# Optimization experiments

Measured on AMD Instinct MI355X. Metric: run time of the kernel, lower is better.

The kernel has to match this reference:

```python
import jax, jax.numpy as jnp
import numpy as np

DN = ('NCHW', 'OIHW', 'NCHW')
EPS = 1e-5

def _conv(x, w, stride, padding):
    return jax.lax.conv_general_dilated(x, w, stride, padding, dimension_numbers=DN)

def _bn(x, g, b, m, v):
    # inference-mode BatchNorm2d
    s = g * jax.lax.rsqrt(v + EPS)
    return x * s[None, :, None, None] + (b - m * s)[None, :, None, None]

def _gn(x, g, b, groups):
    B, C, H, W = x.shape
    xr = x.reshape(B, groups, -1)
    mu = xr.mean(axis=2, keepdims=True)
    var = xr.var(axis=2, keepdims=True)
    xn = ((xr - mu) * jax.lax.rsqrt(var + EPS)).reshape(B, C, H, W)
    return xn * g[None, :, None, None] + b[None, :, None, None]

def _dsconv(f, ow, ob, og, obb, om, ov, w, wb, gg, gb, morph, k=3, extend_scope=1.0):
    B, C, H, W = f.shape
    S = H  # source DSC coordinate map only type-checks for square inputs
    off = jnp.tanh(_bn(_conv(f, ow, (1, 1), [(1, 1), (1, 1)]) + ob[None, :, None, None], og, obb, om, ov))
    # source passes y_offset for morph 0, x_offset for morph 1; both are added to y_new
    sel = off[:, :k] if morph == 0 else off[:, k:]
    center = k // 2
    # _apply_offset: detached clone, center zeroed; cumulative loop is empty for k=3
    off_cum = jax.lax.stop_gradient(sel).at[:, center].set(0.0) * extend_scope
    vals = jnp.linspace(float((-k) // 2), float(k // 2), k, dtype=f.dtype)  # [-2,-0.5,1] for k=3 (source quirk)
    rowc = jnp.arange(S, dtype=f.dtype)[:, None]  # both y_center and x_center equal the row index
    yg = jnp.zeros((k,), f.dtype) if morph == 0 else vals
    xg = vals if morph == 0 else jnp.zeros((k,), f.dtype)
    y = rowc[None, None] + yg[None, :, None, None] + off_cum                       # (B,k,S,S)
    x = jnp.broadcast_to(rowc[None, None] + xg[None, :, None, None], (B, k, S, S))
    rs = lambda t: t.transpose(0, 2, 1, 3).reshape(B, k * S, S)  # b p w h -> b (w p) h
    y, x = rs(y), rs(x)
    y0 = jnp.clip(jnp.floor(y), 0, S - 1); y1 = jnp.clip(jnp.floor(y) + 1.0, 0, S - 1)
    x0 = jnp.clip(jnp.floor(x), 0, S - 1); x1 = jnp.clip(jnp.floor(x) + 1.0, 0, S - 1)
    # source: index_a0 = base_y0 - base + x0  (batch offset cancels -> all batches gather from batch 0)
    flat0 = f[0].transpose(1, 2, 0).reshape(S * S, C)
    gat = lambda yy, xx: flat0[(yy * S + xx).astype(jnp.int32)]  # (B,kS,S,C)
    out = (gat(y0, x0) * ((y1 - y) * (x1 - x))[..., None]
         + gat(y0, x1) * ((y1 - y) * (x - x0))[..., None]
         + gat(y1, x0) * ((y - y0) * (x1 - x))[..., None]
         + gat(y1, x1) * ((y - y0) * (x - x0))[..., None])
    if morph == 0:
        df = out.transpose(0, 3, 1, 2)                    # (B,C,k*S,S)
        z = _conv(df, w, (k, 1), 'VALID')
    else:
        df = out.reshape(B, S, k * S, C).transpose(0, 3, 1, 2)  # (B,C,S,k*S)
        z = _conv(df, w, (1, k), 'VALID')
    z = z + wb[None, :, None, None]
    return jax.nn.silu(_gn(z, gg, gb, w.shape[0] // 4))

def _forward(x, w0, g0, b0, m0, v0,
             owx, obx, ogx, obbx, omx, ovx, wx, bwx, ggx, gbx,
             owy, oby, ogy, obby, omy, ovy, wy, bwy, ggy, gby):
    out0 = jax.nn.silu(_bn(_conv(x, w0, (1, 1), [(1, 1), (1, 1)]), g0, b0, m0, v0))
    outx = _dsconv(x, owx, obx, ogx, obbx, omx, ovx, wx, bwx, ggx, gbx, morph=0)
    outy = _dsconv(x, owy, oby, ogy, obby, omy, ovy, wy, bwy, ggy, gby, morph=1)
    return jnp.concatenate([out0, outx, outy], axis=1)

def setup_inputs() -> dict:
    B, C, O, S, K = 4, 64, 64, 256, 3
    key = jax.random.key(0)
    ks = jax.random.split(key, 32)
    rn = lambda i, sh, sc=1.0: jax.random.normal(ks[i], sh, dtype=jnp.float32) * sc
    ru = lambda i, sh: jax.random.uniform(ks[i], sh, dtype=jnp.float32) + 0.5
    return {
        'x': rn(0, (B, C, S, S)),
        'w0': rn(1, (O, C, 3, 3), 0.05), 'g0': ru(2, (O,)), 'b0': rn(3, (O,), 0.1),
        'm0': rn(4, (O,), 0.1), 'v0': ru(5, (O,)),
        'owx': rn(6, (2 * K, C, 3, 3), 0.05), 'obx': rn(7, (2 * K,), 0.1),
        'ogx': ru(8, (2 * K,)), 'obbx': rn(9, (2 * K,), 0.1), 'omx': rn(10, (2 * K,), 0.1), 'ovx': ru(11, (2 * K,)),
        'wx': rn(12, (O, C, K, 1), 0.05), 'bwx': rn(13, (O,), 0.1), 'ggx': ru(14, (O,)), 'gbx': rn(15, (O,), 0.1),
        'owy': rn(16, (2 * K, C, 3, 3), 0.05), 'oby': rn(17, (2 * K,), 0.1),
        'ogy': ru(18, (2 * K,)), 'obby': rn(19, (2 * K,), 0.1), 'omy': rn(20, (2 * K,), 0.1), 'ovy': ru(21, (2 * K,)),
        'wy': rn(22, (O, C, 1, K), 0.05), 'bwy': rn(23, (O,), 0.1), 'ggy': ru(24, (O,)), 'gby': rn(25, (O,), 0.1),
    }

def reference(x, w0, g0, b0, m0, v0,
              owx, obx, ogx, obbx, omx, ovx, wx, bwx, ggx, gbx,
              owy, oby, ogy, obby, omy, ovy, wy, bwy, ggy, gby):
    return _forward(x, w0, g0, b0, m0, v0,
                    owx, obx, ogx, obbx, omx, ovx, wx, bwx, ggx, gbx,
                    owy, oby, ogy, obby, omy, ovy, wy, bwy, ggy, gby)
```

## Files before the change

### kernel.cpp

```cpp
#include <hip/hip_runtime.h>
#include <hip/hip_bf16.h>
#include <math.h>

#define TS 256
#define HW 65536
#define CIN 64
#define EPSV 1e-5f
#define XPITCH 258

typedef __attribute__((ext_vector_type(8))) short bf16x8;
typedef __attribute__((ext_vector_type(4))) float f32x4;
typedef __attribute__((ext_vector_type(4))) unsigned short u16x4;
typedef unsigned short ushort_t;

__device__ __forceinline__ float silu_f(float v){ return v / (1.0f + expf(-v)); }
__device__ __forceinline__ ushort_t f2bf(float f){
    __hip_bfloat16 h = __float2bfloat16(f);
    return *reinterpret_cast<ushort_t*>(&h);
}
__device__ __forceinline__ float bf2f(ushort_t u){
    unsigned int t = ((unsigned int)u) << 16;
    return __uint_as_float(t);
}

__global__ __launch_bounds__(256) void k_xbf(const float* __restrict__ x, ushort_t* __restrict__ xbf){
    __shared__ float tile[64][65];
    int blk = blockIdx.x;
    int b = blk >> 10;
    int chunk = blk & 1023;
    int p0 = chunk * 64;
    int i = p0 >> 8, jb = p0 & 255;
    int tid = threadIdx.x;
    int lane = tid & 63, grp = tid >> 6;
    #pragma unroll
    for (int k = 0; k < 16; ++k){
        int c = k*4 + grp;
        tile[lane][c] = x[((size_t)(b*CIN + c))*HW + p0 + lane];
    }
    __syncthreads();
    #pragma unroll
    for (int k = 0; k < 16; ++k){
        int pp = k*4 + grp;
        xbf[(((size_t)b*258 + (i+1))*XPITCH + 1 + jb + pp)*64 + lane] = f2bf(tile[pp][lane]);
    }
}

__global__ void k_halo(ushort_t* __restrict__ xbf){
    int r = blockIdx.x;
    int b = blockIdx.y;
    int t = threadIdx.x;
    size_t rowbase = ((size_t)b*258 + r)*XPITCH*64;
    if (r == 0 || r == 257){
        for (int idx = t; idx < XPITCH*64; idx += 256) xbf[rowbase + idx] = 0;
    } else {
        if (t < 64) xbf[rowbase + t] = 0;
        else if (t < 128) xbf[rowbase + (size_t)257*64 + (t-64)] = 0;
    }
}

__global__ __launch_bounds__(256) void k_wrepack(const float* __restrict__ w0, ushort_t* __restrict__ w0bf){
    int idx = blockIdx.x*256 + threadIdx.x;
    int r = idx >> 12;
    int rem = idx & 4095;
    int o = rem >> 6, c = rem & 63;
    w0bf[idx] = f2bf(w0[(o*64 + c)*9 + r]);
}

__global__ __launch_bounds__(256) void k_wdsc(const float* __restrict__ wx, const float* __restrict__ wy,
        ushort_t* __restrict__ wbfx, ushort_t* __restrict__ wbfy){
    int idx = blockIdx.x*256 + threadIdx.x;
    int set = idx / 12288;
    int rem = idx - set*12288;
    int o = rem / 192;
    int k = rem - o*192;
    int t = k >> 6, c = k & 63;
    const float* w = set ? wy : wx;
    ushort_t* dst = set ? wbfy : wbfx;
    dst[rem] = f2bf(w[(o*64 + c)*3 + t]);
}

__global__ __launch_bounds__(256) void k_offp(const float* __restrict__ x,
        const float* __restrict__ owx, const float* __restrict__ owy,
        float* __restrict__ poff){
    __shared__ float xs[8][4][258];
    __shared__ float wsm[4][8][9];
    int by = blockIdx.y;
    int b = by >> 3, chunk = by & 7;
    int i0 = blockIdx.x * 2;
    int tid = threadIdx.x;
    for (int idx = tid; idx < 4*8*9; idx += 256){
        int o = idx / 72;
        int rem = idx - o*72;
        int c = rem / 9, tap = rem - c*9;
        int morph = o >> 1;
        int ch = (o==0)?0:(o==1)?2:(o==2)?3:5;
        const float* w = morph ? owy : owx;
        wsm[o][c][tap] = w[(ch*64 + chunk*8 + c)*9 + tap];
    }
    for (int idx = tid; idx < 8*4*258; idx += 256){
        int c = idx / 1032;
        int rem = idx - c*1032;
        int rr = rem / 258, col = rem - rr*258;
        int gy = i0 + rr - 1, gx = col - 1;
        float v = 0.f;
        if (gy >= 0 && gy < 256 && gx >= 0 && gx < 256)
            v = x[((size_t)(b*64 + chunk*8 + c))*HW + gy*256 + gx];
        xs[c][rr][col] = v;
    }
    __syncthreads();
    float acc[4][2];
    #pragma unroll
    for (int o = 0; o < 4; ++o){ acc[o][0]=0.f; acc[o][1]=0.f; }
    int j = tid;
    #pragma unroll
    for (int c = 0; c < 8; ++c){
        float vrow[4][3];
        #pragma unroll
        for (int rr = 0; rr < 4; ++rr){
            vrow[rr][0] = xs[c][rr][j];
            vrow[rr][1] = xs[c][rr][j+1];
            vrow[rr][2] = xs[c][rr][j+2];
        }
        #pragma unroll
        for (int o = 0; o < 4; ++o){
            const float* wr = wsm[o][c];
            #pragma unroll
            for (int ky = 0; ky < 3; ++ky){
                #pragma unroll
                for (int kx = 0; kx < 3; ++kx){
                    float wv = wr[ky*3+kx];
                    acc[o][0] += wv * vrow[ky][kx];
                    acc[o][1] += wv * vrow[ky+1][kx];
                }
            }
        }
    }
    #pragma unroll
    for (int o = 0; o < 4; ++o){
        size_t base = ((size_t)((chunk*4 + o)*4 + b))*HW;
        poff[base + (size_t)i0*256 + j]     = acc[o][0];
        poff[base + (size_t)(i0+1)*256 + j] = acc[o][1];
    }
}

__global__ __launch_bounds__(256) void k_offred(const float* __restrict__ poff,
        const float* __restrict__ ogx, const float* __restrict__ ovx,
        const float* __restrict__ obx, const float* __restrict__ omx,
        const float* __restrict__ obbx,
        const float* __restrict__ ogy, const float* __restrict__ ovy,
        const float* __restrict__ oby, const float* __restrict__ omy,
        const float* __restrict__ obby,
        float* __restrict__ off0, float* __restrict__ off1){
    int idx = blockIdx.x*256 + threadIdx.x;
    int px = idx & 65535;
    int t2 = idx >> 16;
    int b = t2 & 3;
    int o6 = t2 >> 2;
    if (o6 < 4){
        float s_ = 0.f;
        #pragma unroll
        for (int chunk = 0; chunk < 8; ++chunk)
            s_ += poff[((size_t)((chunk*4 + o6)*4 + b))*HW + px];
        int morph = o6 >> 1;
        int ch = (o6==0)?0:(o6==1)?2:(o6==2)?3:5;
        const float* og_ = morph? ogy:ogx; const float* ov_ = morph? ovy:ovx;
        const float* ob_ = morph? oby:obx; const float* om_ = morph? omy:omx;
        const float* obb_ = morph? obby:obbx;
        float sc = og_[ch]*rsqrtf(ov_[ch]+EPSV);
        float bi = (ob_[ch]-om_[ch])*sc + obb_[ch];
        int pl = (o6 & 1)*2;
        float* dst = (morph? off1:off0) + ((size_t)(b*3+pl))*HW;
        dst[px] = tanhf(s_*sc + bi);
    } else {
        float* dst = ((o6==5)? off1:off0) + ((size_t)(b*3+1))*HW;
        dst[px] = 0.f;
    }
}

__global__ __launch_bounds__(256) void k_conv0_mfma(
        const ushort_t* __restrict__ xbf, const ushort_t* __restrict__ w0bf,
        const float* __restrict__ g0, const float* __restrict__ b0,
        const float* __restrict__ m0, const float* __restrict__ v0,
        float* __restrict__ out){
    __shared__ __align__(16) ushort_t Xs[3*130*64];
    int jh = blockIdx.x;
    int i  = blockIdx.y;
    int b  = blockIdx.z;
    int tid = threadIdx.x;
    int j0h = jh*128;

    int wv = tid >> 6;
    int lane = tid & 63;
    int l15 = lane & 15;
    int lhi = lane >> 4;

    bf16x8 af[18];
    #pragma unroll
    for (int r = 0; r < 9; ++r)
        #pragma unroll
        for (int kc = 0; kc < 2; ++kc)
            af[r*2+kc] = *(const bf16x8*)(w0bf + (size_t)r*4096 + (wv*16 + l15)*64 + kc*32 + lhi*8);

    for (int idx = tid; idx < 3120; idx += 256){
        int rr = idx / 1040;
        int rem = idx - rr*1040;
        int p = rem >> 3, cgrp = rem & 7;
        bf16x8 v = *(const bf16x8*)(xbf + (((size_t)b*258 + (i + rr))*XPITCH + j0h + p)*64 + cgrp*8);
        int byte = rr*16640 + p*128 + ((cgrp*16) ^ ((p & 7) << 4));
        *(bf16x8*)((char*)Xs + byte) = v;
    }
    __syncthreads();

    f32x4 acc[8];
    #pragma unroll
    for (int ni = 0; ni < 8; ++ni) acc[ni] = (f32x4){0.f,0.f,0.f,0.f};

    #pragma unroll
    for (int ni = 0; ni < 8; ++ni){
        #pragma unroll
        for (int r = 0; r < 9; ++r){
            const int rr = r/3, dx = r%3 - 1;
            #pragma unroll
            for (int kc = 0; kc < 2; ++kc){
                int cb = kc*64 + lhi*16;
                int p = ni*16 + l15 + dx + 1;
                bf16x8 bfr = *(const bf16x8*)((char*)Xs + rr*16640 + p*128 + (cb ^ ((p & 7) << 4)));
                acc[ni] = __builtin_amdgcn_mfma_f32_16x16x32_bf16(af[r*2+kc], bfr, acc[ni], 0, 0, 0);
            }
        }
    }
    #pragma unroll
    for (int reg = 0; reg < 4; ++reg){
        int o = wv*16 + lhi*4 + reg;
        float s = g0[o] * rsqrtf(v0[o] + EPSV);
        float bi = b0[o] - m0[o]*s;
        #pragma unroll
        for (int ni = 0; ni < 8; ++ni){
            int j = jh*128 + ni*16 + l15;
            float v = acc[ni][reg]*s + bi;
            out[((size_t)(b*192 + o))*HW + i*TS + j] = silu_f(v);
        }
    }
}

template<int MORPH>
__global__ __launch_bounds__(256) void k_dsc2(const ushort_t* __restrict__ xbf, const float* __restrict__ offm,
        const ushort_t* __restrict__ wbf, const float* __restrict__ wb,
        float* __restrict__ outm, float* __restrict__ part){
    __shared__ __align__(16) ushort_t Vt[3*64*64];
    int b = blockIdx.z;
    int i = blockIdx.y;
    int j0 = blockIdx.x * 64;
    int tid = threadIdx.x;
    int lane16 = tid & 15;
    int pq = tid >> 4;
    const float fi = (float)i;

    #pragma unroll
    for (int it = 0; it < 12; ++it){
        int pair = it*16 + pq;
        int t = pair >> 6, jloc = pair & 63;
        float y, wx1, wx0;
        int x0i, x1i;
        if (MORPH == 0){
            int j = j0 + jloc;
            float off = offm[((size_t)(b*3 + t)*TS + i)*TS + j];
            y = fi + off;
            float vp = (t==0) ? -2.0f : ((t==1) ? -0.5f : 1.0f);
            float xf = fi + vp;
            float x0 = fminf(fmaxf(floorf(xf), 0.f), 255.f);
            float x1 = fminf(fmaxf(floorf(xf) + 1.f, 0.f), 255.f);
            wx1 = x1 - xf; wx0 = xf - x0;
            x0i = (int)x0; x1i = (int)x1;
        } else {
            int q = 3*(j0 + jloc) + t;
            int dl = q >> 8, jj = q & 255;
            float off = offm[((size_t)(b*3 + dl)*TS + i)*TS + jj];
            float vp = (dl==0) ? -2.0f : ((dl==1) ? -0.5f : 1.0f);
            y = fi + vp + off;
            wx1 = (i < 255) ? 1.f : 0.f; wx0 = 0.f;
            x0i = i; x1i = i;
        }
        float yf = floorf(y);
        float y0 = fminf(fmaxf(yf, 0.f), 255.f);
        float y1 = fminf(fmaxf(yf + 1.f, 0.f), 255.f);
        float wy1 = y1 - y, wy0 = y - y0;
        int y0i = (int)y0, y1i = (int)y1;
        int c0 = lane16*4;
        u16x4 a  = *(const u16x4*)(xbf + ((size_t)(y0i+1)*XPITCH + 1 + x0i)*64 + c0);
        u16x4 c_ = *(const u16x4*)(xbf + ((size_t)(y1i+1)*XPITCH + 1 + x0i)*64 + c0);
        float v[4];
        if (MORPH == 0 && wx0 != 0.f){
            u16x4 bv = *(const u16x4*)(xbf + ((size_t)(y0i+1)*XPITCH + 1 + x1i)*64 + c0);
            u16x4 d  = *(const u16x4*)(xbf + ((size_t)(y1i+1)*XPITCH + 1 + x1i)*64 + c0);
            #pragma unroll
            for (int k = 0; k < 4; ++k)
                v[k] = wy1*(wx1*bf2f(a[k]) + wx0*bf2f(bv[k]))
                     + wy0*(wx1*bf2f(c_[k]) + wx0*bf2f(d[k]));
        } else {
            #pragma unroll
            for (int k = 0; k < 4; ++k)
                v[k] = wx1*(wy1*bf2f(a[k]) + wy0*bf2f(c_[k]));
        }
        unsigned int lo = (unsigned int)f2bf(v[0]) | ((unsigned int)f2bf(v[1]) << 16);
        unsigned int hi = (unsigned int)f2bf(v[2]) | ((unsigned int)f2bf(v[3]) << 16);
        int cbyte = (c0*2) ^ ((jloc & 7) << 4);
        uint2 pk; pk.x = lo; pk.y = hi;
        *(uint2*)((char*)Vt + t*8192 + jloc*128 + cbyte) = pk;
    }
    __syncthreads();

    int wv = tid >> 6;
    int lane = tid & 63;
    int l15 = lane & 15, lhi = lane >> 4;
    int mi = wv;
    f32x4 acc[4];
    #pragma unroll
    for (int ni = 0; ni < 4; ++ni) acc[ni] = (f32x4){0.f,0.f,0.f,0.f};
    bf16x8 af[6];
    #pragma unroll
    for (int ks = 0; ks < 6; ++ks)
        af[ks] = *(const bf16x8*)(wbf + (mi*16 + l15)*192 + ks*32 + lhi*8);
    #pragma unroll
    for (int ks = 0; ks < 6; ++ks){
        int t = ks >> 1;
        int cbyte = ((ks & 1)*32 + lhi*8)*2;
        #pragma unroll
        for (int ni = 0; ni < 4; ++ni){
            int j = ni*16 + l15;
            bf16x8 bfr = *(const bf16x8*)((char*)Vt + t*8192 + j*128 + (cbyte ^ ((j & 7) << 4)));
            acc[ni] = __builtin_amdgcn_mfma_f32_16x16x32_bf16(af[ks], bfr, acc[ni], 0, 0, 0);
        }
    }
    float rsum[4], rsq[4];
    #pragma unroll
    for (int reg = 0; reg < 4; ++reg){
        int o = mi*16 + lhi*4 + reg;
        float bias = wb[o];
        float rs = 0.f, rq = 0.f;
        #pragma unroll
        for (int ni = 0; ni < 4; ++ni){
            int j = j0 + ni*16 + l15;
            float val = acc[ni][reg] + bias;
            outm[(size_t)b*192*HW + (size_t)o*HW + i*TS + j] = val;
            rs += val; rq += val*val;
        }
        #pragma unroll
        for (int m = 1; m < 16; m <<= 1){
            rs += __shfl_xor(rs, m, 64);
            rq += __shfl_xor(rq, m, 64);
        }
        rsum[reg] = rs; rsq[reg] = rq;
    }
    if (l15 == 0){
        float ts = rsum[0]+rsum[1]+rsum[2]+rsum[3];
        float tq = rsq[0]+rsq[1]+rsq[2]+rsq[3];
        int g = mi*4 + lhi;
        size_t slot = (((size_t)(MORPH*4 + b)*16 + g)*1024) + (blockIdx.y*4 + blockIdx.x);
        part[slot*2]   = ts;
        part[slot*2+1] = tq;
    }
}

__global__ __launch_bounds__(256) void k_gnfinal2(const float* __restrict__ part, float* __restrict__ stats){
    int slot = blockIdx.x;
    float s = 0.f, q = 0.f;
    for (int k = threadIdx.x; k < 1024; k += 256){
        s += part[((size_t)slot*1024 + k)*2];
        q += part[((size_t)slot*1024 + k)*2 + 1];
    }
    #pragma unroll
    for (int d = 32; d > 0; d >>= 1){ s += __shfl_down(s, d, 64); q += __shfl_down(q, d, 64); }
    __shared__ float rs[4], rq[4];
    int lane = threadIdx.x & 63, wv = threadIdx.x >> 6;
    if (lane == 0){ rs[wv] = s; rq[wv] = q; }
    __syncthreads();
    if (threadIdx.x == 0){
        float S = rs[0]+rs[1]+rs[2]+rs[3];
        float Q = rq[0]+rq[1]+rq[2]+rq[3];
        float inv = 1.f/262144.f;
        float mean = S*inv;
        float var = Q*inv - mean*mean;
        stats[slot*2] = mean;
        stats[slot*2+1] = rsqrtf(var + EPSV);
    }
}

__global__ __launch_bounds__(256) void k_gnapply(float* __restrict__ dout, const float* __restrict__ stats,
        const float* __restrict__ ggx, const float* __restrict__ gbx,
        const float* __restrict__ ggy, const float* __restrict__ gby){
    int idx = blockIdx.x*256 + threadIdx.x;
    int pix4 = idx & 16383;
    int chb = idx >> 14;
    int ch = chb & 127;
    int b = chb >> 7;
    int m = ch >> 6;
    int cc = ch & 63;
    int g = cc >> 2;
    const float* gg = m ? ggy : ggx;
    const float* gb = m ? gby : gbx;
    int si = ((m*4 + b)*16 + g)*2;
    float mean = stats[si], rsig = stats[si+1];
    float sc = rsig * gg[cc];
    float bi = gb[cc] - mean*sc;
    float4* ptr = (float4*)(dout + ((size_t)(b*192 + 64 + ch))*HW) + pix4;
    float4 v = *ptr;
    v.x = silu_f(v.x*sc + bi); v.y = silu_f(v.y*sc + bi);
    v.z = silu_f(v.z*sc + bi); v.w = silu_f(v.w*sc + bi);
    *ptr = v;
}

extern "C" void kernel_launch(void* const* d_in, const int* in_sizes, int n_in,
                              void* d_out, int out_size, void* d_ws, size_t ws_size,
                              hipStream_t stream){
    const float* x    = (const float*)d_in[0];
    const float* w0   = (const float*)d_in[1];
    const float* g0   = (const float*)d_in[2];
    const float* b0   = (const float*)d_in[3];
    const float* m0   = (const float*)d_in[4];
    const float* v0   = (const float*)d_in[5];
    const float* owx  = (const float*)d_in[6];
    const float* obx  = (const float*)d_in[7];
    const float* ogx  = (const float*)d_in[8];
    const float* obbx = (const float*)d_in[9];
    const float* omx  = (const float*)d_in[10];
    const float* ovx  = (const float*)d_in[11];
    const float* wx   = (const float*)d_in[12];
    const float* bwx  = (const float*)d_in[13];
    const float* ggx  = (const float*)d_in[14];
    const float* gbx  = (const float*)d_in[15];
    const float* owy  = (const float*)d_in[16];
    const float* oby  = (const float*)d_in[17];
    const float* ogy  = (const float*)d_in[18];
    const float* obby = (const float*)d_in[19];
    const float* omy  = (const float*)d_in[20];
    const float* ovy  = (const float*)d_in[21];
    const float* wy   = (const float*)d_in[22];
    const float* bwy  = (const float*)d_in[23];
    const float* ggy  = (const float*)d_in[24];
    const float* gby  = (const float*)d_in[25];

    float* out = (float*)d_out;
    ushort_t* xbf  = (ushort_t*)d_ws;
    ushort_t* w0bf = (ushort_t*)((char*)d_ws + 34078464);
    ushort_t* wbfx = (ushort_t*)((char*)d_ws + 34152192);
    ushort_t* wbfy = (ushort_t*)((char*)d_ws + 34176768);
    float* off0  = (float*)((char*)d_ws + 34201344);
    float* off1  = (float*)((char*)d_ws + 37347072);
    float* poff  = (float*)((char*)d_ws + 40492800);
    float* part  = (float*)((char*)d_ws + 40492800);
    float* stats = (float*)((char*)d_ws + 41541376);

    k_xbf<<<4096, 256, 0, stream>>>(x, xbf);
    k_halo<<<dim3(258,4), 256, 0, stream>>>(xbf);
    k_wrepack<<<144, 256, 0, stream>>>(w0, w0bf);
    k_wdsc<<<96, 256, 0, stream>>>(wx, wy, wbfx, wbfy);
    k_offp<<<dim3(128,32), 256, 0, stream>>>(x, owx, owy, poff);
    k_offred<<<6144, 256, 0, stream>>>(poff,
        ogx, ovx, obx, omx, obbx,
        ogy, ovy, oby, omy, obby,
        off0, off1);
    k_conv0_mfma<<<dim3(2,256,4), 256, 0, stream>>>(xbf, w0bf, g0, b0, m0, v0, out);
    k_dsc2<0><<<dim3(4,256,4), 256, 0, stream>>>(xbf, off0, wbfx, bwx, out + (size_t)64*HW, part);
    k_dsc2<1><<<dim3(4,256,4), 256, 0, stream>>>(xbf, off1, wbfy, bwy, out + (size_t)128*HW, part);
    k_gnfinal2<<<128, 256, 0, stream>>>(part, stats);
    k_gnapply<<<32768, 256, 0, stream>>>(out, stats, ggx, gbx, ggy, gby);
}
```

Baseline: 289.0 us.

## Stage DSC conv outputs in bf16 scratch and swizzle conv0 block order

```diff
diff --git a/kernel.cpp b/kernel.cpp
--- a/kernel.cpp
+++ b/kernel.cpp
@@ -183,9 +183,11 @@
         const float* __restrict__ m0, const float* __restrict__ v0,
         float* __restrict__ out){
     __shared__ __align__(16) ushort_t Xs[3*130*64];
-    int jh = blockIdx.x;
-    int i  = blockIdx.y;
-    int b  = blockIdx.z;
+    int id = blockIdx.x;
+    int id2 = ((id & 7) << 8) + (id >> 3);
+    int b  = id2 >> 9;
+    int i  = (id2 >> 1) & 255;
+    int jh = id2 & 1;
     int tid = threadIdx.x;
     int j0h = jh*128;
 
@@ -236,17 +238,17 @@
         float bi = b0[o] - m0[o]*s;
         #pragma unroll
         for (int ni = 0; ni < 8; ++ni){
-            int j = jh*128 + ni*16 + l15;
+            int j = j0h + ni*16 + l15;
             float v = acc[ni][reg]*s + bi;
             out[((size_t)(b*192 + o))*HW + i*TS + j] = silu_f(v);
         }
     }
 }
 
-template<int MORPH>
+template<int MORPH, int ZBF>
 __global__ __launch_bounds__(256) void k_dsc2(const ushort_t* __restrict__ xbf, const float* __restrict__ offm,
         const ushort_t* __restrict__ wbf, const float* __restrict__ wb,
-        float* __restrict__ outm, float* __restrict__ part){
+        float* __restrict__ outm, ushort_t* __restrict__ zb, float* __restrict__ part){
     __shared__ __align__(16) ushort_t Vt[3*64*64];
     int b = blockIdx.z;
     int i = blockIdx.y;
@@ -342,7 +344,10 @@
         for (int ni = 0; ni < 4; ++ni){
             int j = j0 + ni*16 + l15;
             float val = acc[ni][reg] + bias;
-            outm[(size_t)b*192*HW + (size_t)o*HW + i*TS + j] = val;
+            if (ZBF)
+                zb[((size_t)b*64 + o)*HW + i*TS + j] = f2bf(val);
+            else
+                outm[(size_t)b*192*HW + (size_t)o*HW + i*TS + j] = val;
             rs += val; rq += val*val;
         }
         #pragma unroll
@@ -386,7 +391,9 @@
     }
 }
 
-__global__ __launch_bounds__(256) void k_gnapply(float* __restrict__ dout, const float* __restrict__ stats,
+template<int ZBF>
+__global__ __launch_bounds__(256) void k_gnapply(float* __restrict__ dout, const ushort_t* __restrict__ zb,
+        const float* __restrict__ stats,
         const float* __restrict__ ggx, const float* __restrict__ gbx,
         const float* __restrict__ ggy, const float* __restrict__ gby){
     int idx = blockIdx.x*256 + threadIdx.x;
@@ -404,7 +411,13 @@
     float sc = rsig * gg[cc];
     float bi = gb[cc] - mean*sc;
     float4* ptr = (float4*)(dout + ((size_t)(b*192 + 64 + ch))*HW) + pix4;
-    float4 v = *ptr;
+    float4 v;
+    if (ZBF){
+        u16x4 zv = *(const u16x4*)(zb + (((size_t)(m*4 + b)*64 + cc)*HW) + (size_t)pix4*4);
+        v.x = bf2f(zv[0]); v.y = bf2f(zv[1]); v.z = bf2f(zv[2]); v.w = bf2f(zv[3]);
+    } else {
+        v = *ptr;
+    }
     v.x = silu_f(v.x*sc + bi); v.y = silu_f(v.y*sc + bi);
     v.z = silu_f(v.z*sc + bi); v.w = silu_f(v.w*sc + bi);
     *ptr = v;
@@ -448,8 +461,12 @@
     float* off0  = (float*)((char*)d_ws + 34201344);
     float* off1  = (float*)((char*)d_ws + 37347072);
     float* poff  = (float*)((char*)d_ws + 40492800);
-    float* part  = (float*)((char*)d_ws + 40492800);
-    float* stats = (float*)((char*)d_ws + 41541376);
+
+    const size_t ZNEED = 108651264;
+    bool zpath = (ws_size >= ZNEED);
+    ushort_t* zbuf = (ushort_t*)((char*)d_ws + 40492800);
+    float* part  = zpath ? (float*)((char*)d_ws + 107601664) : (float*)((char*)d_ws + 40492800);
+    float* stats = zpath ? (float*)((char*)d_ws + 108650240) : (float*)((char*)d_ws + 41541376);
 
     k_xbf<<<4096, 256, 0, stream>>>(x, xbf);
     k_halo<<<dim3(258,4), 256, 0, stream>>>(xbf);
@@ -460,9 +477,18 @@
         ogx, ovx, obx, omx, obbx,
         ogy, ovy, oby, omy, obby,
         off0, off1);
-    k_conv0_mfma<<<dim3(2,256,4), 256, 0, stream>>>(xbf, w0bf, g0, b0, m0, v0, out);
-    k_dsc2<0><<<dim3(4,256,4), 256, 0, stream>>>(xbf, off0, wbfx, bwx, out + (size_t)64*HW, part);
-    k_dsc2<1><<<dim3(4,256,4), 256, 0, stream>>>(xbf, off1, wbfy, bwy, out + (size_t)128*HW, part);
-    k_gnfinal2<<<128, 256, 0, stream>>>(part, stats);
-    k_gnapply<<<32768, 256, 0, stream>>>(out, stats, ggx, gbx, ggy, gby);
-}
+    k_conv0_mfma<<<2048, 256, 0, stream>>>(xbf, w0bf, g0, b0, m0, v0, out);
+    if (zpath){
+        ushort_t* zb0 = zbuf;
+        ushort_t* zb1 = zbuf + (size_t)4*64*HW;
+        k_dsc2<0,1><<<dim3(4,256,4), 256, 0, stream>>>(xbf, off0, wbfx, bwx, out + (size_t)64*HW, zb0, part);
+        k_dsc2<1,1><<<dim3(4,256,4), 256, 0, stream>>>(xbf, off1, wbfy, bwy, out + (size_t)128*HW, zb1, part);
+        k_gnfinal2<<<128, 256, 0, stream>>>(part, stats);
+        k_gnapply<1><<<32768, 256, 0, stream>>>(out, zbuf, stats, ggx, gbx, ggy, gby);
+    } else {
+        k_dsc2<0,0><<<dim3(4,256,4), 256, 0, stream>>>(xbf, off0, wbfx, bwx, out + (size_t)64*HW, zbuf, part);
+        k_dsc2<1,0><<<dim3(4,256,4), 256, 0, stream>>>(xbf, off1, wbfy, bwy, out + (size_t)128*HW, zbuf, part);
+        k_gnfinal2<<<128, 256, 0, stream>>>(part, stats);
+        k_gnapply<0><<<32768, 256, 0, stream>>>(out, zbuf, stats, ggx, gbx, ggy, gby);
+    }
+}
```

Result: faster. 281.8 us (-2.5%).
